# Performance work log

Hardware: AMD Instinct MI355X
Metric: run time of the kernel (lower is better)

Reference implementation:

```python
import jax, jax.numpy as jnp
import numpy as np

EPS = 1e-8  # undefined global EPS in source; standard small epsilon


def setup_inputs() -> dict:
    key = jax.random.key(0)
    k1, k2 = jax.random.split(key)
    B, C = 262144, 128
    inp = jax.random.uniform(k1, (B, C), dtype=jnp.float32)
    tgt = jax.random.uniform(k2, (B, C), dtype=jnp.float32)
    return {"input": inp, "target": tgt}


def reference(input, target):
    # res = -sum_{i,x} input[i,x] * log(target[i,x] + eps); return [res / B]
    B = input.shape[0]
    res = -jnp.sum(input * jnp.log(target + EPS))
    return jnp.stack([res / B])
```

## Files before the change

### kernel.cpp

```cpp
#include <hip/hip_runtime.h>


typedef float f32x4 __attribute__((ext_vector_type(4)));

constexpr int BLOCK = 256;
constexpr int GRID  = 2048;

__global__ __launch_bounds__(BLOCK, 4) void cce_reduce_kernel(
    const float* __restrict__ inp, const float* __restrict__ tgt,
    float* __restrict__ out, int n4, float neg_inv_b) {
  const f32x4* __restrict__ in4 = reinterpret_cast<const f32x4*>(inp);
  const f32x4* __restrict__ tg4 = reinterpret_cast<const f32x4*>(tgt);

  const int idx    = blockIdx.x * BLOCK + threadIdx.x;
  const int stride = GRID * BLOCK;
  const int step   = 4 * stride;

  float acc0 = 0.f, acc1 = 0.f, acc2 = 0.f, acc3 = 0.f;

#define NTL(P) __builtin_nontemporal_load(P)
#define TERM4(X, Y)                          \
  acc0 += (X)[0] * __logf((Y)[0] + 1e-8f);   \
  acc1 += (X)[1] * __logf((Y)[1] + 1e-8f);   \
  acc2 += (X)[2] * __logf((Y)[2] + 1e-8f);   \
  acc3 += (X)[3] * __logf((Y)[3] + 1e-8f);

  int i = idx;
  if (i + 7 * stride < n4) {
    f32x4 ax0 = in4[i],              ay0 = NTL(tg4 + i);
    f32x4 ax1 = in4[i + stride],     ay1 = NTL(tg4 + i + stride);
    f32x4 ax2 = in4[i + 2 * stride], ay2 = NTL(tg4 + i + 2 * stride);
    f32x4 ax3 = in4[i + 3 * stride], ay3 = NTL(tg4 + i + 3 * stride);
    i += step;

    for (; i + 3 * stride < n4; i += step) {
      f32x4 bx0 = in4[i],              by0 = NTL(tg4 + i);
      f32x4 bx1 = in4[i + stride],     by1 = NTL(tg4 + i + stride);
      f32x4 bx2 = in4[i + 2 * stride], by2 = NTL(tg4 + i + 2 * stride);
      f32x4 bx3 = in4[i + 3 * stride], by3 = NTL(tg4 + i + 3 * stride);
      __builtin_amdgcn_sched_barrier(0);

      TERM4(ax0, ay0) TERM4(ax1, ay1) TERM4(ax2, ay2) TERM4(ax3, ay3)

      ax0 = bx0; ay0 = by0; ax1 = bx1; ay1 = by1;
      ax2 = bx2; ay2 = by2; ax3 = bx3; ay3 = by3;
    }
    TERM4(ax0, ay0) TERM4(ax1, ay1) TERM4(ax2, ay2) TERM4(ax3, ay3)
  }
  for (; i < n4; i += stride) {
    f32x4 x = in4[i], y = NTL(tg4 + i);
    TERM4(x, y)
  }
#undef TERM4
#undef NTL

  float acc = (acc0 + acc1) + (acc2 + acc3);

  #pragma unroll
  for (int off = 32; off > 0; off >>= 1)
    acc += __shfl_down(acc, off, 64);

  __shared__ float s[BLOCK / 64];
  const int lane = threadIdx.x & 63;
  const int wave = threadIdx.x >> 6;
  if (lane == 0) s[wave] = acc;
  __syncthreads();

  if (threadIdx.x == 0) {
    float t = 0.0f;
    #pragma unroll
    for (int w = 0; w < BLOCK / 64; ++w) t += s[w];
    atomicAdd(out, t * neg_inv_b);
  }
}

extern "C" void kernel_launch(void* const* d_in, const int* in_sizes, int n_in,
                              void* d_out, int out_size, void* d_ws, size_t ws_size,
                              hipStream_t stream) {
  const float* inp = reinterpret_cast<const float*>(d_in[0]);
  const float* tgt = reinterpret_cast<const float*>(d_in[1]);
  float* out = reinterpret_cast<float*>(d_out);

  const long long n = (long long)in_sizes[0];
  const int n4 = (int)(n / 4);
  const long long B = 262144;
  const float neg_inv_b = -1.0f / (float)B;

  hipMemsetAsync(d_out, 0, out_size * sizeof(float), stream);

  cce_reduce_kernel<<<GRID, BLOCK, 0, stream>>>(inp, tgt, out, n4, neg_inv_b);
}
```

Measured before the change: 263.7 us.

## Deepen software prefetch pipeline to two stages and halve grid size

The grid-stride reduction loop now keeps two batches of loads in flight (triple-buffered registers) instead of one, so more memory requests are outstanding per thread while the log/multiply work runs. The grid is halved to 1024 blocks, giving each thread more iterations to amortize the deeper prologue and epilogue. The cost is higher register pressure, which could lower occupancy, and fewer waves overall to hide latency.

```diff
diff --git a/kernel.cpp b/kernel.cpp
--- a/kernel.cpp
+++ b/kernel.cpp
@@ -4,7 +4,7 @@
 typedef float f32x4 __attribute__((ext_vector_type(4)));
 
 constexpr int BLOCK = 256;
-constexpr int GRID  = 2048;
+constexpr int GRID  = 1024;
 
 __global__ __launch_bounds__(BLOCK, 4) void cce_reduce_kernel(
     const float* __restrict__ inp, const float* __restrict__ tgt,
@@ -19,39 +19,50 @@
   float acc0 = 0.f, acc1 = 0.f, acc2 = 0.f, acc3 = 0.f;
 
 #define NTL(P) __builtin_nontemporal_load(P)
+#define LOADB(X0, Y0, X1, Y1, X2, Y2, X3, Y3, I)                   \
+  X0 = in4[(I)];                Y0 = NTL(tg4 + (I));               \
+  X1 = in4[(I) + stride];       Y1 = NTL(tg4 + (I) + stride);      \
+  X2 = in4[(I) + 2 * stride];   Y2 = NTL(tg4 + (I) + 2 * stride);  \
+  X3 = in4[(I) + 3 * stride];   Y3 = NTL(tg4 + (I) + 3 * stride);
 #define TERM4(X, Y)                          \
   acc0 += (X)[0] * __logf((Y)[0] + 1e-8f);   \
   acc1 += (X)[1] * __logf((Y)[1] + 1e-8f);   \
   acc2 += (X)[2] * __logf((Y)[2] + 1e-8f);   \
   acc3 += (X)[3] * __logf((Y)[3] + 1e-8f);
+#define COMP(X0, Y0, X1, Y1, X2, Y2, X3, Y3) \
+  TERM4(X0, Y0) TERM4(X1, Y1) TERM4(X2, Y2) TERM4(X3, Y3)
 
   int i = idx;
-  if (i + 7 * stride < n4) {
-    f32x4 ax0 = in4[i],              ay0 = NTL(tg4 + i);
-    f32x4 ax1 = in4[i + stride],     ay1 = NTL(tg4 + i + stride);
-    f32x4 ax2 = in4[i + 2 * stride], ay2 = NTL(tg4 + i + 2 * stride);
-    f32x4 ax3 = in4[i + 3 * stride], ay3 = NTL(tg4 + i + 3 * stride);
-    i += step;
+  if (i + 11 * stride < n4) {
+    f32x4 ax0, ay0, ax1, ay1, ax2, ay2, ax3, ay3;
+    f32x4 bx0, by0, bx1, by1, bx2, by2, bx3, by3;
+    f32x4 cx0, cy0, cx1, cy1, cx2, cy2, cx3, cy3;
+
+    LOADB(ax0, ay0, ax1, ay1, ax2, ay2, ax3, ay3, i)
+    LOADB(bx0, by0, bx1, by1, bx2, by2, bx3, by3, i + step)
+    i += 2 * step;
 
     for (; i + 3 * stride < n4; i += step) {
-      f32x4 bx0 = in4[i],              by0 = NTL(tg4 + i);
-      f32x4 bx1 = in4[i + stride],     by1 = NTL(tg4 + i + stride);
-      f32x4 bx2 = in4[i + 2 * stride], by2 = NTL(tg4 + i + 2 * stride);
-      f32x4 bx3 = in4[i + 3 * stride], by3 = NTL(tg4 + i + 3 * stride);
+      LOADB(cx0, cy0, cx1, cy1, cx2, cy2, cx3, cy3, i)
       __builtin_amdgcn_sched_barrier(0);
 
-      TERM4(ax0, ay0) TERM4(ax1, ay1) TERM4(ax2, ay2) TERM4(ax3, ay3)
+      COMP(ax0, ay0, ax1, ay1, ax2, ay2, ax3, ay3)
 
       ax0 = bx0; ay0 = by0; ax1 = bx1; ay1 = by1;
       ax2 = bx2; ay2 = by2; ax3 = bx3; ay3 = by3;
+      bx0 = cx0; by0 = cy0; bx1 = cx1; by1 = cy1;
+      bx2 = cx2; by2 = cy2; bx3 = cx3; by3 = cy3;
     }
-    TERM4(ax0, ay0) TERM4(ax1, ay1) TERM4(ax2, ay2) TERM4(ax3, ay3)
+    COMP(ax0, ay0, ax1, ay1, ax2, ay2, ax3, ay3)
+    COMP(bx0, by0, bx1, by1, bx2, by2, bx3, by3)
   }
   for (; i < n4; i += stride) {
     f32x4 x = in4[i], y = NTL(tg4 + i);
     TERM4(x, y)
   }
+#undef COMP
 #undef TERM4
+#undef LOADB
 #undef NTL
 
   float acc = (acc0 + acc1) + (acc2 + acc3);
```

Result: no change. 263.4 us (-0.1%).
